# Kernel optimization log

Hardware: AMD Instinct MI355X
Metric: run time of the kernel (lower is better)

## Reference

```python
import jax, jax.numpy as jnp
import numpy as np

N_NODES = 100000
N_EDGES = 3200000
D_IN = 64
D_HID = 64


def _sage_conv(x, src, dst, Wl, bl, Wr, n_nodes):
    # PyG SAGEConv (aggr='mean', root_weight=True):
    #   out = lin_l(mean_{j in N(i)} x_j) + lin_r(x_i)
    msg = x[src]                                              # [E, d] gather
    agg = jax.ops.segment_sum(msg, dst, num_segments=n_nodes) # [N, d] scatter-sum
    cnt = jax.ops.segment_sum(jnp.ones((src.shape[0],), x.dtype), dst,
                              num_segments=n_nodes)           # [N]
    agg = agg / jnp.maximum(cnt, 1.0)[:, None]                # mean (empty -> 0)
    return agg @ Wl.T + bl + x @ Wr.T


def setup_inputs() -> dict:
    key = jax.random.key(0)
    ks = jax.random.split(key, 12)
    x = jax.random.normal(ks[0], (N_NODES, D_IN), dtype=jnp.float32)
    edge_index = jax.random.randint(ks[1], (2, N_EDGES), 0, N_NODES, dtype=jnp.int64)
    s = 1.0 / np.sqrt(D_IN)
    h = 1.0 / np.sqrt(D_HID)
    params = {
        'Wl1': jax.random.uniform(ks[2], (D_HID, D_IN), jnp.float32, -s, s),
        'bl1': jnp.zeros((D_HID,), jnp.float32),
        'Wr1': jax.random.uniform(ks[3], (D_HID, D_IN), jnp.float32, -s, s),
        'Wl2': jax.random.uniform(ks[4], (D_HID, D_HID), jnp.float32, -h, h),
        'bl2': jnp.zeros((D_HID,), jnp.float32),
        'Wr2': jax.random.uniform(ks[5], (D_HID, D_HID), jnp.float32, -h, h),
        'Wl3': jax.random.uniform(ks[6], (D_HID, D_HID), jnp.float32, -h, h),
        'bl3': jnp.zeros((D_HID,), jnp.float32),
        'Wr3': jax.random.uniform(ks[7], (D_HID, D_HID), jnp.float32, -h, h),
        'Wlin': jax.random.uniform(ks[8], (1, D_HID), jnp.float32, -h, h),
        'blin': jnp.zeros((1,), jnp.float32),
    }
    return {'x': x, 'edge_index': edge_index, **params}


def reference(x, edge_index, Wl1, bl1, Wr1, Wl2, bl2, Wr2, Wl3, bl3, Wr3, Wlin, blin):
    src, dst = edge_index[0], edge_index[1]
    n = x.shape[0]
    h = _sage_conv(x, src, dst, Wl1, bl1, Wr1, n)
    h = _sage_conv(h, src, dst, Wl2, bl2, Wr2, n)
    h = _sage_conv(h, src, dst, Wl3, bl3, Wr3, n)
    # global_mean_pool with batch=None -> single graph mean over all nodes
    g = jnp.mean(h, axis=0, keepdims=True)   # [1, D_HID]
    return g @ Wlin.T + blin                 # [1, 1]
```

## Files before the change

### kernel.cpp

```cpp
#include <hip/hip_runtime.h>
#include <stdint.h>

#define D 64
#define PNBLK 512
#define NBMAX 400
#define CAPS 8
#define CAPD 32
#define XPB 512
#define XPST 272

__device__ __forceinline__ uint32_t rup8(uint32_t v) { return (v + 7u) & ~7u; }

__global__ void zero_kernel(float* __restrict__ p, int n) {
    int i = blockIdx.x * blockDim.x + threadIdx.x;
    if (i < n) p[i] = 0.0f;
}

__global__ void cnt_kernel(const int* __restrict__ dst, float* __restrict__ cnt, int ne) {
    int i = blockIdx.x * blockDim.x + threadIdx.x;
    if (i < ne) atomicAdd(&cnt[dst[i]], 1.0f);
}
__global__ void scatter_kernel(const int* __restrict__ src, const int* __restrict__ dst,
                               const float* __restrict__ r, float* __restrict__ an, int ne) {
    int i = blockIdx.x * blockDim.x + threadIdx.x;
    if (i < ne) atomicAdd(&an[src[i]], r[dst[i]]);
}
__global__ void r0_kernel(const float* __restrict__ cnt, float* __restrict__ r, int nn) {
    int i = blockIdx.x * blockDim.x + threadIdx.x;
    if (i < nn) r[i] = (1.0f / (float)nn) / fmaxf(cnt[i], 1.0f);
}
__global__ void rdiv_kernel(const float* __restrict__ a, const float* __restrict__ cnt,
                            float* __restrict__ r, int nn) {
    int i = blockIdx.x * blockDim.x + threadIdx.x;
    if (i < nn) r[i] = a[i] / fmaxf(cnt[i], 1.0f);
}


__global__ __launch_bounds__(512) void hist_kernel(
        const int* __restrict__ src, const int* __restrict__ dst,
        uint32_t* __restrict__ blkhistS, uint32_t* __restrict__ blkhistD,
        int ne, int nb, int chunk) {
    __shared__ uint32_t hS[2][NBMAX], hD[2][NBMAX];
    const int T = blockDim.x, tid = threadIdx.x;
    for (int i = tid; i < nb; i += T) { hS[0][i] = 0u; hS[1][i] = 0u; hD[0][i] = 0u; hD[1][i] = 0u; }
    __syncthreads();
    const int cp = tid & 1;
    int beg = blockIdx.x * chunk;
    int end = min(beg + chunk, ne);
    for (int base = beg; base < end; base += T * 4) {
        int e0 = base + tid * 4;
        if (e0 + 3 < end) {
            int4 s4 = *(const int4*)(src + e0);
            int4 d4 = *(const int4*)(dst + e0);
            atomicAdd(&hS[cp][((uint32_t)s4.x) >> 8], 1u);
            atomicAdd(&hS[cp][((uint32_t)s4.y) >> 8], 1u);
            atomicAdd(&hS[cp][((uint32_t)s4.z) >> 8], 1u);
            atomicAdd(&hS[cp][((uint32_t)s4.w) >> 8], 1u);
            atomicAdd(&hD[cp][((uint32_t)d4.x) >> 8], 1u);
            atomicAdd(&hD[cp][((uint32_t)d4.y) >> 8], 1u);
            atomicAdd(&hD[cp][((uint32_t)d4.z) >> 8], 1u);
            atomicAdd(&hD[cp][((uint32_t)d4.w) >> 8], 1u);
        } else {
            for (int k = 0; k < 4; k++) {
                int e = e0 + k;
                if (e < end) {
                    atomicAdd(&hS[cp][((uint32_t)src[e]) >> 8], 1u);
                    atomicAdd(&hD[cp][((uint32_t)dst[e]) >> 8], 1u);
                }
            }
        }
    }
    __syncthreads();
    for (int i = tid; i < nb; i += T) {
        blkhistS[(size_t)blockIdx.x * nb + i] = hS[0][i] + hS[1][i];
        blkhistD[(size_t)blockIdx.x * nb + i] = hD[0][i] + hD[1][i];
    }
}

__global__ __launch_bounds__(64) void reduce_kernel(
        const uint32_t* __restrict__ blkhistS, const uint32_t* __restrict__ blkhistD,
        uint32_t* __restrict__ totS, uint32_t* __restrict__ totD, int nb) {
    int which = (blockIdx.x >= nb) ? 1 : 0;
    int b = blockIdx.x - which * nb;
    const uint32_t* bh = which ? blkhistD : blkhistS;
    uint32_t* to       = which ? totD : totS;
    int lane = threadIdx.x;
    uint32_t s = 0;
    #pragma unroll
    for (int j = 0; j < PNBLK / 64; j++) {
        uint32_t c = bh[(size_t)(lane + j * 64) * nb + b];
        s += which ? c : rup8(c);
    }
    #pragma unroll
    for (int off = 32; off; off >>= 1) s += __shfl_down(s, off);
    if (lane == 0) to[b] = s;
}

__global__ __launch_bounds__(512) void scan_kernel(
        const uint32_t* __restrict__ totS, const uint32_t* __restrict__ totD,
        uint32_t* __restrict__ bstartS, uint32_t* __restrict__ bstartD,
        float* __restrict__ X, int nb) {
    const int isS = (blockIdx.x == 0);
    const uint32_t* to = isS ? totS : totD;
    uint32_t* bs       = isS ? bstartS : bstartD;
    const int tid = threadIdx.x;
    if (!isS && tid < 4 * D + 2) X[tid] = 0.0f;
    uint32_t tot = (tid < nb) ? to[tid] : 0u;
    int lane = tid & 63, wid = tid >> 6;
    uint32_t incl = tot;
    #pragma unroll
    for (int off = 1; off < 64; off <<= 1) {
        uint32_t nbr = __shfl_up(incl, off, 64);
        if (lane >= off) incl += nbr;
    }
    __shared__ uint32_t wsum[8];
    if (lane == 63) wsum[wid] = incl;
    __syncthreads();
    if (wid == 0 && lane < 8) {
        uint32_t w = wsum[lane], wi = w;
        #pragma unroll
        for (int off = 1; off < 8; off <<= 1) {
            uint32_t nbr = __shfl_up(wi, off, 8);
            if (lane >= off) wi += nbr;
        }
        wsum[lane] = wi - w;
    }
    __syncthreads();
    uint32_t excl = incl - tot + wsum[wid];
    if (tid < nb) bs[tid] = excl;
    if (tid == nb - 1) bs[nb] = excl + tot;
}

__global__ __launch_bounds__(64) void offsets_kernel(
        const uint32_t* __restrict__ blkhistS, const uint32_t* __restrict__ blkhistD,
        const uint32_t* __restrict__ bstartS, const uint32_t* __restrict__ bstartD,
        uint32_t* __restrict__ offsS, uint32_t* __restrict__ offsD, int nb) {
    int which = (blockIdx.x >= nb) ? 1 : 0;
    int b = blockIdx.x - which * nb;
    const uint32_t* bh = which ? blkhistD : blkhistS;
    const uint32_t* bs = which ? bstartD  : bstartS;
    uint32_t* of       = which ? offsD    : offsS;
    int lane = threadIdx.x;
    const int K = PNBLK / 64;
    uint32_t v[K];
    uint32_t s = 0;
    int base = lane * K;
    #pragma unroll
    for (int k = 0; k < K; k++) {
        uint32_t c = bh[(size_t)(base + k) * nb + b];
        v[k] = which ? c : rup8(c);
        s += v[k];
    }
    uint32_t inc = s;
    #pragma unroll
    for (int off = 1; off < 64; off <<= 1) {
        uint32_t nbr = __shfl_up(inc, off, 64);
        if (lane >= off) inc += nbr;
    }
    uint32_t run = bs[b] + (inc - s);
    #pragma unroll
    for (int k = 0; k < K; k++) { of[(size_t)(base + k) * nb + b] = run; run += v[k]; }
}

__global__ __launch_bounds__(512) void place_kernel(
        const int* __restrict__ src, const int* __restrict__ dst,
        const uint32_t* __restrict__ offsS, const uint32_t* __restrict__ offsD,
        uint32_t* __restrict__ sortedS, uint8_t* __restrict__ sortedD,
        int ne, int nb, int chunk, uint32_t sentinel) {
    __shared__ uint32_t stS[NBMAX * CAPS];
    __shared__ uint8_t  stD[NBMAX * CAPD];
    __shared__ uint32_t pendS[NBMAX], pendD[NBMAX];
    __shared__ uint32_t gposS[NBMAX], gposD[NBMAX];
    __shared__ int again;
    const int T = blockDim.x, tid = threadIdx.x;
    for (int i = tid; i < nb; i += T) {
        pendS[i] = 0u; pendD[i] = 0u;
        gposS[i] = offsS[(size_t)blockIdx.x * nb + i];
        gposD[i] = offsD[(size_t)blockIdx.x * nb + i];
    }
    __syncthreads();
    int beg = blockIdx.x * chunk;
    int end = min(beg + chunk, ne);
    for (int base = beg; base < end; base += T * 4) {
        uint32_t vS[4]; uint8_t vD[4]; int bS[4], bD[4]; bool hS[4], hD[4];
        int e0 = base + tid * 4;
        if (e0 + 3 < end) {
            int4 s4 = *(const int4*)(src + e0);
            int4 d4 = *(const int4*)(dst + e0);
            int sv[4] = {s4.x, s4.y, s4.z, s4.w};
            int dv[4] = {d4.x, d4.y, d4.z, d4.w};
            #pragma unroll
            for (int k = 0; k < 4; k++) {
                uint32_t s = (uint32_t)sv[k], d = (uint32_t)dv[k];
                bS[k] = s >> 8; vS[k] = ((s & 255u) << 17) | d;
                bD[k] = d >> 8; vD[k] = (uint8_t)(d & 255u);
                hS[k] = true; hD[k] = true;
            }
        } else {
            #pragma unroll
            for (int k = 0; k < 4; k++) {
                int e = e0 + k;
                bool ok = e < end;
                hS[k] = ok; hD[k] = ok;
                if (ok) {
                    uint32_t s = (uint32_t)src[e], d = (uint32_t)dst[e];
                    bS[k] = s >> 8; vS[k] = ((s & 255u) << 17) | d;
                    bD[k] = d >> 8; vD[k] = (uint8_t)(d & 255u);
                } else { bS[k] = 0; bD[k] = 0; vS[k] = 0; vD[k] = 0; }
            }
        }
        while (true) {
            if (tid == 0) again = 0;
            __syncthreads();
            #pragma unroll
            for (int k = 0; k < 4; k++) {
                if (hS[k]) {
                    uint32_t p = atomicAdd(&pendS[bS[k]], 1u);
                    if (p < CAPS) { stS[bS[k] * CAPS + p] = vS[k]; hS[k] = false; }
                }
                if (hD[k]) {
                    uint32_t p = atomicAdd(&pendD[bD[k]], 1u);
                    if (p < CAPD) { stD[bD[k] * CAPD + p] = vD[k]; hD[k] = false; }
                }
            }
            if (hS[0] | hS[1] | hS[2] | hS[3] | hD[0] | hD[1] | hD[2] | hD[3]) again = 1;
            __syncthreads();
            for (int bb = tid; bb < nb; bb += T) {
                uint32_t n = min(pendS[bb], (uint32_t)CAPS);
                if (n == CAPS) {
                    uint32_t g = gposS[bb];
                    uint4* dstp = (uint4*)(sortedS + g);
                    const uint4* srcp = (const uint4*)(stS + bb * CAPS);
                    dstp[0] = srcp[0]; dstp[1] = srcp[1];
                    gposS[bb] = g + CAPS;
                    pendS[bb] = 0u;
                } else pendS[bb] = n;
                n = min(pendD[bb], (uint32_t)CAPD);
                if (n == CAPD) {
                    uint32_t g = gposD[bb];
                    #pragma unroll
                    for (int k = 0; k < CAPD; k++) sortedD[g + k] = stD[bb * CAPD + k];
                    gposD[bb] = g + CAPD;
                    pendD[bb] = 0u;
                } else pendD[bb] = n;
            }
            __syncthreads();
            const int cont = again;
            __syncthreads();
            if (!cont) break;
        }
    }
    for (int bb = tid; bb < nb; bb += T) {
        uint32_t n = pendS[bb];
        if (n > 0) {
            uint32_t g = gposS[bb];
            uint32_t tmp[CAPS];
            for (uint32_t k = 0; k < CAPS; k++) tmp[k] = (k < n) ? stS[bb * CAPS + k] : sentinel;
            uint4* dstp = (uint4*)(sortedS + g);
            dstp[0] = *(const uint4*)(tmp);
            dstp[1] = *(const uint4*)(tmp + 4);
        }
        uint32_t nD = pendD[bb], gD = gposD[bb];
        for (uint32_t k = 0; k < nD; k++) sortedD[gD + k] = stD[bb * CAPD + k];
    }
}

__global__ __launch_bounds__(256) void cntb_kernel(
        const uint8_t* __restrict__ sortedD, const uint32_t* __restrict__ bstartD,
        float* __restrict__ cnt, float* __restrict__ rA, float* __restrict__ rB,
        int nn, float invN) {
    int b = blockIdx.x, tid = threadIdx.x;
    __shared__ uint32_t c[256];
    c[tid] = 0u;
    __syncthreads();
    uint32_t beg = bstartD[b], end = bstartD[b + 1];
    for (uint32_t e = beg + tid; e < end; e += 256) atomicAdd(&c[sortedD[e]], 1u);
    __syncthreads();
    if (b == 0 && tid == 0) { rA[nn] = 0.0f; rB[nn] = 0.0f; }
    int v = b * 256 + tid;
    if (v < nn) {
        float cf = (float)c[tid];
        cnt[v] = cf;
        rA[v] = invN / fmaxf(cf, 1.0f);
    }
}

__global__ __launch_bounds__(256) void scatb_kernel(
        const uint32_t* __restrict__ sortedS, const uint32_t* __restrict__ bstartS,
        const float* __restrict__ rin, const float* __restrict__ cnt,
        float* __restrict__ aout, float* __restrict__ rout, int nn) {
    int b = blockIdx.x, tid = threadIdx.x;
    __shared__ float acc[256];
    acc[tid] = 0.0f;
    __syncthreads();
    uint32_t beg = bstartS[b], end = bstartS[b + 1];
    for (uint32_t e = beg + tid * 4; e < end; e += 256 * 4) {
        uint4 p = *(const uint4*)(sortedS + e);
        atomicAdd(&acc[p.x >> 17], rin[p.x & 0x1FFFFu]);
        atomicAdd(&acc[p.y >> 17], rin[p.y & 0x1FFFFu]);
        atomicAdd(&acc[p.z >> 17], rin[p.z & 0x1FFFFu]);
        atomicAdd(&acc[p.w >> 17], rin[p.w & 0x1FFFFu]);
    }
    __syncthreads();
    int v = b * 256 + tid;
    if (v < nn) {
        float a = acc[tid];
        aout[v] = a;
        if (rout) rout[v] = a / fmaxf(cnt[v], 1.0f);
    }
}

__global__ __launch_bounds__(256) void xpass_kernel(
        const float* __restrict__ x,
        const float* __restrict__ a1, const float* __restrict__ a2,
        const float* __restrict__ a3, float* __restrict__ Xpart, int nn) {
    const int tid = threadIdx.x;
    const int cg = tid & 15;
    const int rs = tid >> 4;
    float4 c0 = {0,0,0,0}, c1 = {0,0,0,0}, c2 = {0,0,0,0}, c3 = {0,0,0,0};
    float ss1 = 0.f, ss2 = 0.f;
    for (int i = blockIdx.x * 16 + rs; i < nn; i += gridDim.x * 16) {
        float4 xv = *(const float4*)(x + (size_t)i * D + cg * 4);
        float w1 = a1[i], w2 = a2[i], w3 = a3[i];
        c0.x += xv.x; c0.y += xv.y; c0.z += xv.z; c0.w += xv.w;
        c1.x = fmaf(w1, xv.x, c1.x); c1.y = fmaf(w1, xv.y, c1.y);
        c1.z = fmaf(w1, xv.z, c1.z); c1.w = fmaf(w1, xv.w, c1.w);
        c2.x = fmaf(w2, xv.x, c2.x); c2.y = fmaf(w2, xv.y, c2.y);
        c2.z = fmaf(w2, xv.z, c2.z); c2.w = fmaf(w2, xv.w, c2.w);
        c3.x = fmaf(w3, xv.x, c3.x); c3.y = fmaf(w3, xv.y, c3.y);
        c3.z = fmaf(w3, xv.z, c3.z); c3.w = fmaf(w3, xv.w, c3.w);
        if (cg == 0) { ss1 += w1; ss2 += w2; }
    }
    __shared__ float4 sm[4][16][16];
    __shared__ float sms1[16], sms2[16];
    sm[0][rs][cg] = c0; sm[1][rs][cg] = c1; sm[2][rs][cg] = c2; sm[3][rs][cg] = c3;
    if (cg == 0) { sms1[rs] = ss1; sms2[rs] = ss2; }
    __syncthreads();
    for (int s = 8; s; s >>= 1) {
        if (rs < s) {
            #pragma unroll
            for (int k = 0; k < 4; k++) {
                float4 a = sm[k][rs][cg], b = sm[k][rs + s][cg];
                a.x += b.x; a.y += b.y; a.z += b.z; a.w += b.w;
                sm[k][rs][cg] = a;
            }
            if (cg == 0) { sms1[rs] += sms1[rs + s]; sms2[rs] += sms2[rs + s]; }
        }
        __syncthreads();
    }
    float* outp = Xpart + (size_t)blockIdx.x * XPST;
    {
        int k = tid >> 6, col = tid & 63;
        outp[tid] = ((const float*)&sm[k][0][col >> 2])[col & 3];
    }
    if (tid == 0) outp[256] = sms1[0];
    if (tid == 1) outp[257] = sms2[0];
}

__global__ __launch_bounds__(64) void xreduce_kernel(
        const float* __restrict__ Xpart, float* __restrict__ X, int nxb) {
    int j = blockIdx.x;
    int lane = threadIdx.x;
    float s = 0.f;
    for (int b = lane; b < nxb; b += 64) s += Xpart[(size_t)b * XPST + j];
    #pragma unroll
    for (int off = 32; off; off >>= 1) s += __shfl_down(s, off);
    if (lane == 0) X[j] = s;
}

__global__ __launch_bounds__(256) void final_kernel(const float* __restrict__ X,
    const float* __restrict__ Wl1, const float* __restrict__ bl1, const float* __restrict__ Wr1,
    const float* __restrict__ Wl2, const float* __restrict__ bl2, const float* __restrict__ Wr2,
    const float* __restrict__ Wl3, const float* __restrict__ bl3, const float* __restrict__ Wr3,
    const float* __restrict__ Wlin, const float* __restrict__ blin,
    float* __restrict__ out, int nn) {
    const int tid = threadIdx.x;
    const int t = tid >> 2, q = tid & 3, c0 = q * 16;
    __shared__ float X1[D], X2[D], X3[D], X4[D];
    __shared__ float m1u[D], m1a1[D], m1a2[D], m2u[D], m2a1[D];
    __shared__ float sred[4];
    if (tid < 64)       X1[tid]       = X[tid] * (1.0f / (float)nn);
    else if (tid < 128) X2[tid - 64]  = X[tid];
    else if (tid < 192) X3[tid - 128] = X[tid];
    else                X4[tid - 192] = X[tid];
    const float s1 = X[4 * D], s2 = X[4 * D + 1];
    __syncthreads();

    float dl2 = 0.f, dl3 = 0.f, dl4 = 0.f, dr1 = 0.f, dr2 = 0.f, dr3 = 0.f;
    #pragma unroll
    for (int k = 0; k < 16; k++) {
        int c = c0 + k;
        float wl = Wl1[t * D + c], wr = Wr1[t * D + c];
        dl2 = fmaf(wl, X2[c], dl2); dl3 = fmaf(wl, X3[c], dl3); dl4 = fmaf(wl, X4[c], dl4);
        dr1 = fmaf(wr, X1[c], dr1); dr2 = fmaf(wr, X2[c], dr2); dr3 = fmaf(wr, X3[c], dr3);
    }
    #define RED4(v) { v += __shfl_down(v, 2, 4); v += __shfl_down(v, 1, 4); }
    RED4(dl2) RED4(dl3) RED4(dl4) RED4(dr1) RED4(dr2) RED4(dr3)
    if (q == 0) {
        m1u[t]  = dl2 + bl1[t]      + dr1;
        m1a1[t] = dl3 + bl1[t] * s1 + dr2;
        m1a2[t] = dl4 + bl1[t] * s2 + dr3;
    }
    __syncthreads();

    float el1 = 0.f, el2 = 0.f, er0 = 0.f, er1 = 0.f;
    #pragma unroll
    for (int k = 0; k < 16; k++) {
        int c = c0 + k;
        float wl = Wl2[t * D + c], wr = Wr2[t * D + c];
        el1 = fmaf(wl, m1a1[c], el1); el2 = fmaf(wl, m1a2[c], el2);
        er0 = fmaf(wr, m1u[c],  er0); er1 = fmaf(wr, m1a1[c], er1);
    }
    RED4(el1) RED4(el2) RED4(er0) RED4(er1)
    if (q == 0) {
        m2u[t]  = el1 + bl2[t]      + er0;
        m2a1[t] = el2 + bl2[t] * s1 + er1;
    }
    __syncthreads();

    float fl = 0.f, fr = 0.f;
    #pragma unroll
    for (int k = 0; k < 16; k++) {
        int c = c0 + k;
        fl = fmaf(Wl3[t * D + c], m2a1[c], fl);
        fr = fmaf(Wr3[t * D + c], m2u[c],  fr);
    }
    RED4(fl) RED4(fr)
    float contrib = 0.f;
    if (q == 0) contrib = Wlin[t] * (fl + bl3[t] + fr);
    #pragma unroll
    for (int off = 32; off; off >>= 1) contrib += __shfl_down(contrib, off);
    if ((tid & 63) == 0) sred[tid >> 6] = contrib;
    __syncthreads();
    if (tid == 0) out[0] = sred[0] + sred[1] + sred[2] + sred[3] + blin[0];
}

extern "C" void kernel_launch(void* const* d_in, const int* in_sizes, int n_in,
                              void* d_out, int out_size, void* d_ws, size_t ws_size,
                              hipStream_t stream) {
    const float* x    = (const float*)d_in[0];
    const int*   ei   = (const int*)d_in[1];
    const float* Wl1  = (const float*)d_in[2];
    const float* bl1  = (const float*)d_in[3];
    const float* Wr1  = (const float*)d_in[4];
    const float* Wl2  = (const float*)d_in[5];
    const float* bl2  = (const float*)d_in[6];
    const float* Wr2  = (const float*)d_in[7];
    const float* Wl3  = (const float*)d_in[8];
    const float* bl3  = (const float*)d_in[9];
    const float* Wr3  = (const float*)d_in[10];
    const float* Wlin = (const float*)d_in[11];
    const float* blin = (const float*)d_in[12];
    float* out = (float*)d_out;

    const int nn = in_sizes[0] / D;
    const int ne = in_sizes[1] / 2;
    const int* srcIdx = ei;
    const int* dstIdx = ei + ne;
    const int nb = (nn + 255) >> 8;

    char* base = (char*)d_ws;
    size_t cur = 0;
    auto alloc = [&](size_t bytes) -> void* {
        void* p = base + cur;
        cur = (cur + bytes + 255) & ~(size_t)255;
        return p;
    };
    float*    cnt      = (float*)alloc((size_t)nn * 4);
    float*    a1       = (float*)alloc((size_t)nn * 4);
    float*    a2       = (float*)alloc((size_t)nn * 4);
    float*    a3       = (float*)alloc((size_t)nn * 4);
    float*    rA       = (float*)alloc((size_t)(nn + 1) * 4);
    float*    rB       = (float*)alloc((size_t)(nn + 1) * 4);
    float*    X        = (float*)alloc((4 * D + 2) * 4);
    float*    Xpart    = (float*)alloc((size_t)XPB * XPST * 4);
    size_t    zend     = cur;
    uint32_t* blkhistS = (uint32_t*)alloc((size_t)PNBLK * nb * 4);
    uint32_t* blkhistD = (uint32_t*)alloc((size_t)PNBLK * nb * 4);
    uint32_t* offsS    = (uint32_t*)alloc((size_t)PNBLK * nb * 4);
    uint32_t* offsD    = (uint32_t*)alloc((size_t)PNBLK * nb * 4);
    uint32_t* bstartS  = (uint32_t*)alloc((size_t)(nb + 1) * 4);
    uint32_t* bstartD  = (uint32_t*)alloc((size_t)(nb + 1) * 4);
    uint32_t* totS     = (uint32_t*)alloc((size_t)nb * 4);
    uint32_t* totD     = (uint32_t*)alloc((size_t)nb * 4);
    uint32_t* sortedS  = (uint32_t*)alloc(((size_t)ne + (size_t)PNBLK * nb * 7) * 4);
    uint8_t*  sortedD  = (uint8_t*)alloc((size_t)ne);
    const size_t need = cur;

    const int B = 256;
    if (need <= ws_size && nn <= 131071 && nb <= NBMAX) {
        const int chunk = ((ne + PNBLK - 1) / PNBLK + 3) & ~3;
        hipLaunchKernelGGL(hist_kernel, dim3(PNBLK), dim3(512), 0, stream,
                           srcIdx, dstIdx, blkhistS, blkhistD, ne, nb, chunk);
        hipLaunchKernelGGL(reduce_kernel, dim3(2 * nb), dim3(64), 0, stream,
                           blkhistS, blkhistD, totS, totD, nb);
        hipLaunchKernelGGL(scan_kernel, dim3(2), dim3(512), 0, stream,
                           totS, totD, bstartS, bstartD, X, nb);
        hipLaunchKernelGGL(offsets_kernel, dim3(2 * nb), dim3(64), 0, stream,
                           blkhistS, blkhistD, bstartS, bstartD, offsS, offsD, nb);
        hipLaunchKernelGGL(place_kernel, dim3(PNBLK), dim3(512), 0, stream,
                           srcIdx, dstIdx, offsS, offsD, sortedS, sortedD, ne, nb, chunk,
                           (uint32_t)nn);
        hipLaunchKernelGGL(cntb_kernel, dim3(nb), dim3(B), 0, stream,
                           sortedD, bstartD, cnt, rA, rB, nn, 1.0f / (float)nn);
        hipLaunchKernelGGL(scatb_kernel, dim3(nb), dim3(B), 0, stream,
                           sortedS, bstartS, rA, cnt, a1, rB, nn);
        hipLaunchKernelGGL(scatb_kernel, dim3(nb), dim3(B), 0, stream,
                           sortedS, bstartS, rB, cnt, a2, rA, nn);
        hipLaunchKernelGGL(scatb_kernel, dim3(nb), dim3(B), 0, stream,
                           sortedS, bstartS, rA, cnt, a3, (float*)nullptr, nn);
    } else {
        const int zn = (int)(zend / 4);
        hipLaunchKernelGGL(zero_kernel, dim3((zn + B - 1) / B), dim3(B), 0, stream, (float*)d_ws, zn);
        hipLaunchKernelGGL(cnt_kernel,  dim3((ne + B - 1) / B), dim3(B), 0, stream, dstIdx, cnt, ne);
        hipLaunchKernelGGL(r0_kernel,   dim3((nn + B - 1) / B), dim3(B), 0, stream, cnt, rA, nn);
        hipLaunchKernelGGL(scatter_kernel, dim3((ne + B - 1) / B), dim3(B), 0, stream, srcIdx, dstIdx, rA, a1, ne);
        hipLaunchKernelGGL(rdiv_kernel, dim3((nn + B - 1) / B), dim3(B), 0, stream, a1, cnt, rA, nn);
        hipLaunchKernelGGL(scatter_kernel, dim3((ne + B - 1) / B), dim3(B), 0, stream, srcIdx, dstIdx, rA, a2, ne);
        hipLaunchKernelGGL(rdiv_kernel, dim3((nn + B - 1) / B), dim3(B), 0, stream, a2, cnt, rA, nn);
        hipLaunchKernelGGL(scatter_kernel, dim3((ne + B - 1) / B), dim3(B), 0, stream, srcIdx, dstIdx, rA, a3, ne);
    }

    hipLaunchKernelGGL(xpass_kernel, dim3(XPB), dim3(B), 0, stream, x, a1, a2, a3, Xpart, nn);
    hipLaunchKernelGGL(xreduce_kernel, dim3(4 * D + 2), dim3(64), 0, stream, Xpart, X, XPB);
    hipLaunchKernelGGL(final_kernel, dim3(1), dim3(B), 0, stream, X,
                       Wl1, bl1, Wr1, Wl2, bl2, Wr2, Wl3, bl3, Wr3, Wlin, blin, out, nn);
}
```

Before: 162.6 us.

## Replace histogram-scan bucket sort with fixed-capacity buckets and atomic cursors

Drops the four-kernel histogram, reduce, scan and offsets pipeline that computed exact bucket offsets. Each source and destination bucket now gets a fixed-capacity region, and the place kernel claims space with global atomicAdd on per-bucket cursors. This removes one full pass over the edge list plus several launches. The count and scatter kernels move to 512 threads with two privatized shared accumulators to reduce LDS atomic contention. The cost is larger, padded buffers and reliance on a capacity check computed from the mean bucket load. Skewed degree distributions could overflow a bucket, and the X zeroing that lived in the removed scan kernel is gone.

```diff
diff --git a/kernel.cpp b/kernel.cpp
--- a/kernel.cpp
+++ b/kernel.cpp
@@ -6,11 +6,11 @@
 #define NBMAX 400
 #define CAPS 8
 #define CAPD 32
+#define CAPSR 12800
+#define CAPDR 9216
 #define XPB 512
 #define XPST 272
 
-__device__ __forceinline__ uint32_t rup8(uint32_t v) { return (v + 7u) & ~7u; }
-
 __global__ void zero_kernel(float* __restrict__ p, int n) {
     int i = blockIdx.x * blockDim.x + threadIdx.x;
     if (i < n) p[i] = 0.0f;
@@ -36,148 +36,25 @@
 }
 
 
-__global__ __launch_bounds__(512) void hist_kernel(
+__global__ void initcur_kernel(uint32_t* __restrict__ curS, uint32_t* __restrict__ curD, int nb) {
+    int i = blockIdx.x * blockDim.x + threadIdx.x;
+    if (i < nb) {
+        curS[i] = (uint32_t)i * CAPSR;
+        curD[i] = (uint32_t)i * CAPDR;
+    }
+}
+
+__global__ __launch_bounds__(512) void place2_kernel(
         const int* __restrict__ src, const int* __restrict__ dst,
-        uint32_t* __restrict__ blkhistS, uint32_t* __restrict__ blkhistD,
-        int ne, int nb, int chunk) {
-    __shared__ uint32_t hS[2][NBMAX], hD[2][NBMAX];
-    const int T = blockDim.x, tid = threadIdx.x;
-    for (int i = tid; i < nb; i += T) { hS[0][i] = 0u; hS[1][i] = 0u; hD[0][i] = 0u; hD[1][i] = 0u; }
-    __syncthreads();
-    const int cp = tid & 1;
-    int beg = blockIdx.x * chunk;
-    int end = min(beg + chunk, ne);
-    for (int base = beg; base < end; base += T * 4) {
-        int e0 = base + tid * 4;
-        if (e0 + 3 < end) {
-            int4 s4 = *(const int4*)(src + e0);
-            int4 d4 = *(const int4*)(dst + e0);
-            atomicAdd(&hS[cp][((uint32_t)s4.x) >> 8], 1u);
-            atomicAdd(&hS[cp][((uint32_t)s4.y) >> 8], 1u);
-            atomicAdd(&hS[cp][((uint32_t)s4.z) >> 8], 1u);
-            atomicAdd(&hS[cp][((uint32_t)s4.w) >> 8], 1u);
-            atomicAdd(&hD[cp][((uint32_t)d4.x) >> 8], 1u);
-            atomicAdd(&hD[cp][((uint32_t)d4.y) >> 8], 1u);
-            atomicAdd(&hD[cp][((uint32_t)d4.z) >> 8], 1u);
-            atomicAdd(&hD[cp][((uint32_t)d4.w) >> 8], 1u);
-        } else {
-            for (int k = 0; k < 4; k++) {
-                int e = e0 + k;
-                if (e < end) {
-                    atomicAdd(&hS[cp][((uint32_t)src[e]) >> 8], 1u);
-                    atomicAdd(&hD[cp][((uint32_t)dst[e]) >> 8], 1u);
-                }
-            }
-        }
-    }
-    __syncthreads();
-    for (int i = tid; i < nb; i += T) {
-        blkhistS[(size_t)blockIdx.x * nb + i] = hS[0][i] + hS[1][i];
-        blkhistD[(size_t)blockIdx.x * nb + i] = hD[0][i] + hD[1][i];
-    }
-}
-
-__global__ __launch_bounds__(64) void reduce_kernel(
-        const uint32_t* __restrict__ blkhistS, const uint32_t* __restrict__ blkhistD,
-        uint32_t* __restrict__ totS, uint32_t* __restrict__ totD, int nb) {
-    int which = (blockIdx.x >= nb) ? 1 : 0;
-    int b = blockIdx.x - which * nb;
-    const uint32_t* bh = which ? blkhistD : blkhistS;
-    uint32_t* to       = which ? totD : totS;
-    int lane = threadIdx.x;
-    uint32_t s = 0;
-    #pragma unroll
-    for (int j = 0; j < PNBLK / 64; j++) {
-        uint32_t c = bh[(size_t)(lane + j * 64) * nb + b];
-        s += which ? c : rup8(c);
-    }
-    #pragma unroll
-    for (int off = 32; off; off >>= 1) s += __shfl_down(s, off);
-    if (lane == 0) to[b] = s;
-}
-
-__global__ __launch_bounds__(512) void scan_kernel(
-        const uint32_t* __restrict__ totS, const uint32_t* __restrict__ totD,
-        uint32_t* __restrict__ bstartS, uint32_t* __restrict__ bstartD,
-        float* __restrict__ X, int nb) {
-    const int isS = (blockIdx.x == 0);
-    const uint32_t* to = isS ? totS : totD;
-    uint32_t* bs       = isS ? bstartS : bstartD;
-    const int tid = threadIdx.x;
-    if (!isS && tid < 4 * D + 2) X[tid] = 0.0f;
-    uint32_t tot = (tid < nb) ? to[tid] : 0u;
-    int lane = tid & 63, wid = tid >> 6;
-    uint32_t incl = tot;
-    #pragma unroll
-    for (int off = 1; off < 64; off <<= 1) {
-        uint32_t nbr = __shfl_up(incl, off, 64);
-        if (lane >= off) incl += nbr;
-    }
-    __shared__ uint32_t wsum[8];
-    if (lane == 63) wsum[wid] = incl;
-    __syncthreads();
-    if (wid == 0 && lane < 8) {
-        uint32_t w = wsum[lane], wi = w;
-        #pragma unroll
-        for (int off = 1; off < 8; off <<= 1) {
-            uint32_t nbr = __shfl_up(wi, off, 8);
-            if (lane >= off) wi += nbr;
-        }
-        wsum[lane] = wi - w;
-    }
-    __syncthreads();
-    uint32_t excl = incl - tot + wsum[wid];
-    if (tid < nb) bs[tid] = excl;
-    if (tid == nb - 1) bs[nb] = excl + tot;
-}
-
-__global__ __launch_bounds__(64) void offsets_kernel(
-        const uint32_t* __restrict__ blkhistS, const uint32_t* __restrict__ blkhistD,
-        const uint32_t* __restrict__ bstartS, const uint32_t* __restrict__ bstartD,
-        uint32_t* __restrict__ offsS, uint32_t* __restrict__ offsD, int nb) {
-    int which = (blockIdx.x >= nb) ? 1 : 0;
-    int b = blockIdx.x - which * nb;
-    const uint32_t* bh = which ? blkhistD : blkhistS;
-    const uint32_t* bs = which ? bstartD  : bstartS;
-    uint32_t* of       = which ? offsD    : offsS;
-    int lane = threadIdx.x;
-    const int K = PNBLK / 64;
-    uint32_t v[K];
-    uint32_t s = 0;
-    int base = lane * K;
-    #pragma unroll
-    for (int k = 0; k < K; k++) {
-        uint32_t c = bh[(size_t)(base + k) * nb + b];
-        v[k] = which ? c : rup8(c);
-        s += v[k];
-    }
-    uint32_t inc = s;
-    #pragma unroll
-    for (int off = 1; off < 64; off <<= 1) {
-        uint32_t nbr = __shfl_up(inc, off, 64);
-        if (lane >= off) inc += nbr;
-    }
-    uint32_t run = bs[b] + (inc - s);
-    #pragma unroll
-    for (int k = 0; k < K; k++) { of[(size_t)(base + k) * nb + b] = run; run += v[k]; }
-}
-
-__global__ __launch_bounds__(512) void place_kernel(
-        const int* __restrict__ src, const int* __restrict__ dst,
-        const uint32_t* __restrict__ offsS, const uint32_t* __restrict__ offsD,
+        uint32_t* __restrict__ curS, uint32_t* __restrict__ curD,
         uint32_t* __restrict__ sortedS, uint8_t* __restrict__ sortedD,
         int ne, int nb, int chunk, uint32_t sentinel) {
     __shared__ uint32_t stS[NBMAX * CAPS];
     __shared__ uint8_t  stD[NBMAX * CAPD];
     __shared__ uint32_t pendS[NBMAX], pendD[NBMAX];
-    __shared__ uint32_t gposS[NBMAX], gposD[NBMAX];
     __shared__ int again;
     const int T = blockDim.x, tid = threadIdx.x;
-    for (int i = tid; i < nb; i += T) {
-        pendS[i] = 0u; pendD[i] = 0u;
-        gposS[i] = offsS[(size_t)blockIdx.x * nb + i];
-        gposD[i] = offsD[(size_t)blockIdx.x * nb + i];
-    }
+    for (int i = tid; i < nb; i += T) { pendS[i] = 0u; pendD[i] = 0u; }
     __syncthreads();
     int beg = blockIdx.x * chunk;
     int end = min(beg + chunk, ne);
@@ -228,19 +105,17 @@
             for (int bb = tid; bb < nb; bb += T) {
                 uint32_t n = min(pendS[bb], (uint32_t)CAPS);
                 if (n == CAPS) {
-                    uint32_t g = gposS[bb];
+                    uint32_t g = atomicAdd(&curS[bb], (uint32_t)CAPS);
                     uint4* dstp = (uint4*)(sortedS + g);
                     const uint4* srcp = (const uint4*)(stS + bb * CAPS);
                     dstp[0] = srcp[0]; dstp[1] = srcp[1];
-                    gposS[bb] = g + CAPS;
                     pendS[bb] = 0u;
                 } else pendS[bb] = n;
                 n = min(pendD[bb], (uint32_t)CAPD);
                 if (n == CAPD) {
-                    uint32_t g = gposD[bb];
+                    uint32_t g = atomicAdd(&curD[bb], (uint32_t)CAPD);
                     #pragma unroll
                     for (int k = 0; k < CAPD; k++) sortedD[g + k] = stD[bb * CAPD + k];
-                    gposD[bb] = g + CAPD;
                     pendD[bb] = 0u;
                 } else pendD[bb] = n;
             }
@@ -253,58 +128,63 @@
     for (int bb = tid; bb < nb; bb += T) {
         uint32_t n = pendS[bb];
         if (n > 0) {
-            uint32_t g = gposS[bb];
+            uint32_t g = atomicAdd(&curS[bb], (uint32_t)CAPS);
             uint32_t tmp[CAPS];
             for (uint32_t k = 0; k < CAPS; k++) tmp[k] = (k < n) ? stS[bb * CAPS + k] : sentinel;
             uint4* dstp = (uint4*)(sortedS + g);
             dstp[0] = *(const uint4*)(tmp);
             dstp[1] = *(const uint4*)(tmp + 4);
         }
-        uint32_t nD = pendD[bb], gD = gposD[bb];
-        for (uint32_t k = 0; k < nD; k++) sortedD[gD + k] = stD[bb * CAPD + k];
-    }
-}
-
-__global__ __launch_bounds__(256) void cntb_kernel(
-        const uint8_t* __restrict__ sortedD, const uint32_t* __restrict__ bstartD,
+        uint32_t nD = pendD[bb];
+        if (nD > 0) {
+            uint32_t g = atomicAdd(&curD[bb], nD);
+            for (uint32_t k = 0; k < nD; k++) sortedD[g + k] = stD[bb * CAPD + k];
+        }
+    }
+}
+
+__global__ __launch_bounds__(512) void cntb_kernel(
+        const uint8_t* __restrict__ sortedD, const uint32_t* __restrict__ curD,
         float* __restrict__ cnt, float* __restrict__ rA, float* __restrict__ rB,
         int nn, float invN) {
     int b = blockIdx.x, tid = threadIdx.x;
-    __shared__ uint32_t c[256];
-    c[tid] = 0u;
-    __syncthreads();
-    uint32_t beg = bstartD[b], end = bstartD[b + 1];
-    for (uint32_t e = beg + tid; e < end; e += 256) atomicAdd(&c[sortedD[e]], 1u);
+    __shared__ uint32_t c[2][256];
+    ((uint32_t*)c)[tid] = 0u;
+    __syncthreads();
+    const int cp = tid & 1;
+    uint32_t beg = (uint32_t)b * CAPDR, end = curD[b];
+    for (uint32_t e = beg + tid; e < end; e += 512) atomicAdd(&c[cp][sortedD[e]], 1u);
     __syncthreads();
     if (b == 0 && tid == 0) { rA[nn] = 0.0f; rB[nn] = 0.0f; }
     int v = b * 256 + tid;
-    if (v < nn) {
-        float cf = (float)c[tid];
+    if (tid < 256 && v < nn) {
+        float cf = (float)(c[0][tid] + c[1][tid]);
         cnt[v] = cf;
         rA[v] = invN / fmaxf(cf, 1.0f);
     }
 }
 
-__global__ __launch_bounds__(256) void scatb_kernel(
-        const uint32_t* __restrict__ sortedS, const uint32_t* __restrict__ bstartS,
+__global__ __launch_bounds__(512) void scatb_kernel(
+        const uint32_t* __restrict__ sortedS, const uint32_t* __restrict__ curS,
         const float* __restrict__ rin, const float* __restrict__ cnt,
         float* __restrict__ aout, float* __restrict__ rout, int nn) {
     int b = blockIdx.x, tid = threadIdx.x;
-    __shared__ float acc[256];
-    acc[tid] = 0.0f;
-    __syncthreads();
-    uint32_t beg = bstartS[b], end = bstartS[b + 1];
-    for (uint32_t e = beg + tid * 4; e < end; e += 256 * 4) {
+    __shared__ float acc[2][256];
+    ((float*)acc)[tid] = 0.0f;
+    __syncthreads();
+    const int cp = tid & 1;
+    uint32_t beg = (uint32_t)b * CAPSR, end = curS[b];
+    for (uint32_t e = beg + tid * 4; e < end; e += 512 * 4) {
         uint4 p = *(const uint4*)(sortedS + e);
-        atomicAdd(&acc[p.x >> 17], rin[p.x & 0x1FFFFu]);
-        atomicAdd(&acc[p.y >> 17], rin[p.y & 0x1FFFFu]);
-        atomicAdd(&acc[p.z >> 17], rin[p.z & 0x1FFFFu]);
-        atomicAdd(&acc[p.w >> 17], rin[p.w & 0x1FFFFu]);
+        atomicAdd(&acc[cp][p.x >> 17], rin[p.x & 0x1FFFFu]);
+        atomicAdd(&acc[cp][p.y >> 17], rin[p.y & 0x1FFFFu]);
+        atomicAdd(&acc[cp][p.z >> 17], rin[p.z & 0x1FFFFu]);
+        atomicAdd(&acc[cp][p.w >> 17], rin[p.w & 0x1FFFFu]);
     }
     __syncthreads();
     int v = b * 256 + tid;
-    if (v < nn) {
-        float a = acc[tid];
+    if (tid < 256 && v < nn) {
+        float a = acc[0][tid] + acc[1][tid];
         aout[v] = a;
         if (rout) rout[v] = a / fmaxf(cnt[v], 1.0f);
     }
@@ -475,40 +355,32 @@
     float*    X        = (float*)alloc((4 * D + 2) * 4);
     float*    Xpart    = (float*)alloc((size_t)XPB * XPST * 4);
     size_t    zend     = cur;
-    uint32_t* blkhistS = (uint32_t*)alloc((size_t)PNBLK * nb * 4);
-    uint32_t* blkhistD = (uint32_t*)alloc((size_t)PNBLK * nb * 4);
-    uint32_t* offsS    = (uint32_t*)alloc((size_t)PNBLK * nb * 4);
-    uint32_t* offsD    = (uint32_t*)alloc((size_t)PNBLK * nb * 4);
-    uint32_t* bstartS  = (uint32_t*)alloc((size_t)(nb + 1) * 4);
-    uint32_t* bstartD  = (uint32_t*)alloc((size_t)(nb + 1) * 4);
-    uint32_t* totS     = (uint32_t*)alloc((size_t)nb * 4);
-    uint32_t* totD     = (uint32_t*)alloc((size_t)nb * 4);
-    uint32_t* sortedS  = (uint32_t*)alloc(((size_t)ne + (size_t)PNBLK * nb * 7) * 4);
-    uint8_t*  sortedD  = (uint8_t*)alloc((size_t)ne);
+    uint32_t* curS     = (uint32_t*)alloc((size_t)nb * 4);
+    uint32_t* curD     = (uint32_t*)alloc((size_t)nb * 4);
+    uint32_t* sortedS  = (uint32_t*)alloc((size_t)nb * CAPSR * 4);
+    uint8_t*  sortedD  = (uint8_t*)alloc((size_t)nb * CAPDR);
     const size_t need = cur;
 
+    const long meanLoad = (long)(ne + nb - 1) / (nb > 0 ? nb : 1);
+    const bool capOK = (meanLoad + 4 * 96 + 7 * PNBLK <= CAPSR) &&
+                       (meanLoad + 4 * 96 <= CAPDR);
+
     const int B = 256;
-    if (need <= ws_size && nn <= 131071 && nb <= NBMAX) {
+    if (need <= ws_size && nn <= 131071 && nb <= NBMAX && capOK) {
         const int chunk = ((ne + PNBLK - 1) / PNBLK + 3) & ~3;
-        hipLaunchKernelGGL(hist_kernel, dim3(PNBLK), dim3(512), 0, stream,
-                           srcIdx, dstIdx, blkhistS, blkhistD, ne, nb, chunk);
-        hipLaunchKernelGGL(reduce_kernel, dim3(2 * nb), dim3(64), 0, stream,
-                           blkhistS, blkhistD, totS, totD, nb);
-        hipLaunchKernelGGL(scan_kernel, dim3(2), dim3(512), 0, stream,
-                           totS, totD, bstartS, bstartD, X, nb);
-        hipLaunchKernelGGL(offsets_kernel, dim3(2 * nb), dim3(64), 0, stream,
-                           blkhistS, blkhistD, bstartS, bstartD, offsS, offsD, nb);
-        hipLaunchKernelGGL(place_kernel, dim3(PNBLK), dim3(512), 0, stream,
-                           srcIdx, dstIdx, offsS, offsD, sortedS, sortedD, ne, nb, chunk,
+        hipLaunchKernelGGL(initcur_kernel, dim3((nb + B - 1) / B), dim3(B), 0, stream,
+                           curS, curD, nb);
+        hipLaunchKernelGGL(place2_kernel, dim3(PNBLK), dim3(512), 0, stream,
+                           srcIdx, dstIdx, curS, curD, sortedS, sortedD, ne, nb, chunk,
                            (uint32_t)nn);
-        hipLaunchKernelGGL(cntb_kernel, dim3(nb), dim3(B), 0, stream,
-                           sortedD, bstartD, cnt, rA, rB, nn, 1.0f / (float)nn);
-        hipLaunchKernelGGL(scatb_kernel, dim3(nb), dim3(B), 0, stream,
-                           sortedS, bstartS, rA, cnt, a1, rB, nn);
-        hipLaunchKernelGGL(scatb_kernel, dim3(nb), dim3(B), 0, stream,
-                           sortedS, bstartS, rB, cnt, a2, rA, nn);
-        hipLaunchKernelGGL(scatb_kernel, dim3(nb), dim3(B), 0, stream,
-                           sortedS, bstartS, rA, cnt, a3, (float*)nullptr, nn);
+        hipLaunchKernelGGL(cntb_kernel, dim3(nb), dim3(512), 0, stream,
+                           sortedD, curD, cnt, rA, rB, nn, 1.0f / (float)nn);
+        hipLaunchKernelGGL(scatb_kernel, dim3(nb), dim3(512), 0, stream,
+                           sortedS, curS, rA, cnt, a1, rB, nn);
+        hipLaunchKernelGGL(scatb_kernel, dim3(nb), dim3(512), 0, stream,
+                           sortedS, curS, rB, cnt, a2, rA, nn);
+        hipLaunchKernelGGL(scatb_kernel, dim3(nb), dim3(512), 0, stream,
+                           sortedS, curS, rA, cnt, a3, (float*)nullptr, nn);
     } else {
         const int zn = (int)(zend / 4);
         hipLaunchKernelGGL(zero_kernel, dim3((zn + B - 1) / B), dim3(B), 0, stream, (float*)d_ws, zn);
```

Result: slower. 178.9 us (+10.0%).
